# Performance work log

Hardware: AMD Instinct MI355X
Metric: run time of the kernel (lower is better)

Reference implementation:

```python
import jax, jax.numpy as jnp
import numpy as np

NUM_BANDS = 8
WINDOW = 2048
OVERLAP = 1024
SR = 16000


def _band_mask(L):
    # Replicates torch: band = searchsorted(band_ranges, |freq|, left) - 1.
    # DC bin gives band=-1 which torch negative-indexes into the LAST band,
    # hence the mod. All bins satisfy band < NUM_BANDS, so all are assigned.
    freqs = np.fft.fftfreq(L, 1.0 / SR)
    ranges = np.linspace(0.0, SR / 2.0, NUM_BANDS + 1)
    idx = np.searchsorted(ranges, np.abs(freqs), side='left') - 1
    idx = idx % NUM_BANDS
    mask = (idx[None, :] == np.arange(NUM_BANDS)[:, None]).astype(np.float32)
    return jnp.asarray(mask)  # [bands, L]


def _band_signals(x):
    # mag*exp(i*phase) of masked bins == masked complex bins; ifft().real per band
    L = x.shape[-1]
    X = jnp.fft.fft(x)                         # [B, L] complex
    mask = _band_mask(L)                       # [bands, L]
    Xb = X[:, None, :] * mask[None, :, :]      # [B, bands, L]
    return jnp.fft.ifft(Xb).real               # [B, bands, L]


def _chunks(sig):
    L = sig.shape[-1]
    hop = WINDOW - OVERLAP
    n = (L - OVERLAP) // hop                   # num_chunks (static)
    idx = (jnp.arange(n) * hop)[:, None] + jnp.arange(WINDOW)[None, :]  # [n, W]
    return sig[:, :, idx]                       # [B, bands, n, W]


def _loudness(x):
    # BS.1770-style energy loudness (vectorized stand-in for the repo's
    # undefined `loudness` helper): -0.691 + 10*log10(mean square)
    ms = jnp.mean(x * x, axis=-1)
    return -0.691 + 10.0 * jnp.log10(ms + 1e-12)


def reference(watermarked_signals, original_signals):
    ro = _band_signals(original_signals)
    rw = _band_signals(watermarked_signals)
    lo = _loudness(_chunks(ro))                # [B, bands, n]
    lw = _loudness(_chunks(rw))
    lo = jnp.where(jnp.isnan(lo), 0.0, lo)
    lw = jnp.where(jnp.isnan(lw), 0.0, lw)
    diff = (lw - lo).reshape(-1)               # ordered (i, j, k) like the torch loop
    w = jax.nn.softmax(diff)
    return jnp.sum(w * diff)


def setup_inputs() -> dict:
    key = jax.random.key(0)
    k1, k2 = jax.random.split(key)
    B, L = 8, 160000
    return {
        'watermarked_signals': jax.random.normal(k1, (B, L), dtype=jnp.float32),
        'original_signals': jax.random.normal(k2, (B, L), dtype=jnp.float32),
    }
```

## Files before the change

kernel.cpp:

```cpp
#include <hip/hip_runtime.h>
#include <math.h>

constexpr int L      = 160000;
constexpr int BATCH  = 8;
constexpr int NB     = 8;
constexpr int NHOPS  = 156;
constexpr int NCHUNK = 155;
constexpr int RS     = 289;
constexpr float TWO_PI = 6.28318530717958647692f;

__device__ __forceinline__ float2 cmulf(float2 a, float2 b) {
  return make_float2(a.x * b.x - a.y * b.y, a.x * b.y + a.y * b.x);
}

__device__ __forceinline__ float2 cisf(float a) {
  float s, c;
  __sincosf(a, &s, &c);
  return make_float2(c, s);
}

__device__ __forceinline__ int pad8(int i) { return i + (i >> 3); }

template <int SIGN>
__device__ __forceinline__ void bf4s(float2* v) {
  float2 t0 = make_float2(v[0].x + v[2].x, v[0].y + v[2].y);
  float2 t1 = make_float2(v[0].x - v[2].x, v[0].y - v[2].y);
  float2 t2 = make_float2(v[1].x + v[3].x, v[1].y + v[3].y);
  float2 t3 = make_float2(v[1].x - v[3].x, v[1].y - v[3].y);
  v[0] = make_float2(t0.x + t2.x, t0.y + t2.y);
  v[2] = make_float2(t0.x - t2.x, t0.y - t2.y);
  if constexpr (SIGN < 0) {
    v[1] = make_float2(t1.x + t3.y, t1.y - t3.x);
    v[3] = make_float2(t1.x - t3.y, t1.y + t3.x);
  } else {
    v[1] = make_float2(t1.x - t3.y, t1.y + t3.x);
    v[3] = make_float2(t1.x + t3.y, t1.y - t3.x);
  }
}

template <int SIGN>
__device__ __forceinline__ void bf5s(float2* v) {
  const float c1 = 0.30901699437494745f, s1 = 0.9510565162951535f;
  const float c2 = -0.8090169943749475f, s2 = 0.5877852522924731f;
  float2 t1 = make_float2(v[1].x + v[4].x, v[1].y + v[4].y);
  float2 t3 = make_float2(v[1].x - v[4].x, v[1].y - v[4].y);
  float2 t2 = make_float2(v[2].x + v[3].x, v[2].y + v[3].y);
  float2 t4 = make_float2(v[2].x - v[3].x, v[2].y - v[3].y);
  float2 a = make_float2(v[0].x + c1 * t1.x + c2 * t2.x, v[0].y + c1 * t1.y + c2 * t2.y);
  float2 b = make_float2(s1 * t3.x + s2 * t4.x, s1 * t3.y + s2 * t4.y);
  float2 c = make_float2(v[0].x + c2 * t1.x + c1 * t2.x, v[0].y + c2 * t1.y + c1 * t2.y);
  float2 d = make_float2(s2 * t3.x - s1 * t4.x, s2 * t3.y - s1 * t4.y);
  v[0] = make_float2(v[0].x + t1.x + t2.x, v[0].y + t1.y + t2.y);
  if constexpr (SIGN < 0) {
    v[1] = make_float2(a.x + b.y, a.y - b.x);
    v[4] = make_float2(a.x - b.y, a.y + b.x);
    v[2] = make_float2(c.x + d.y, c.y - d.x);
    v[3] = make_float2(c.x - d.y, c.y + d.x);
  } else {
    v[1] = make_float2(a.x - b.y, a.y + b.x);
    v[4] = make_float2(a.x + b.y, a.y - b.x);
    v[2] = make_float2(c.x - d.y, c.y + d.x);
    v[3] = make_float2(c.x + d.y, c.y - d.x);
  }
}

template <int R>
__device__ __forceinline__ void twchain(float2* v, float2 t1) {
  float2 t = t1;
  v[1] = cmulf(v[1], t);
#pragma unroll
  for (int r = 2; r < R; ++r) { t = cmulf(t, t1); v[r] = cmulf(v[r], t); }
}

__device__ __forceinline__ int rev3_5(int q) {
  int q5 = q / 5, q25 = q / 25;
  int d0 = q - 5 * q5, d1 = q5 - 5 * q25;
  return 25 * d0 + 5 * d1 + q25;
}

__device__ __forceinline__ int rev3_4(int q) {
  return ((q & 3) << 4) | (q & 12) | (q >> 4);
}

template <int SUB, int SIGN>
__device__ __forceinline__ void dif5_ip_stage_c(float2* a, int ln) {
  int i1 = ln, i2 = ln + 64;
  bool g2 = (i2 < 125);
  int j1 = i1 % SUB, j2 = i2 % SUB;
  int b1 = (i1 / SUB) * (5 * SUB) + j1;
  int b2 = (i2 / SUB) * (5 * SUB) + j2;
  float2 u[5], v[5];
#pragma unroll
  for (int r = 0; r < 5; ++r) u[r] = a[b1 + SUB * r];
  if (g2) {
#pragma unroll
    for (int r = 0; r < 5; ++r) v[r] = a[b2 + SUB * r];
  }
  bf5s<SIGN>(u);
  twchain<5>(u, cisf((float)SIGN * (TWO_PI / (float)(5 * SUB)) * (float)j1));
  if (g2) {
    bf5s<SIGN>(v);
    twchain<5>(v, cisf((float)SIGN * (TWO_PI / (float)(5 * SUB)) * (float)j2));
  }
#pragma unroll
  for (int r = 0; r < 5; ++r) a[b1 + SUB * r] = u[r];
  if (g2) {
#pragma unroll
    for (int r = 0; r < 5; ++r) a[b2 + SUB * r] = v[r];
  }
}

template <int SUB>
__device__ __forceinline__ void dif5_ip_stage_t(float2* a, int ln, float2 t1a, float2 t1b) {
  int i1 = ln, i2 = ln + 64;
  bool g2 = (i2 < 125);
  int j1 = i1 % SUB, j2 = i2 % SUB;
  int b1 = (i1 / SUB) * (5 * SUB) + j1;
  int b2 = (i2 / SUB) * (5 * SUB) + j2;
  float2 u[5], v[5];
#pragma unroll
  for (int r = 0; r < 5; ++r) u[r] = a[b1 + SUB * r];
  if (g2) {
#pragma unroll
    for (int r = 0; r < 5; ++r) v[r] = a[b2 + SUB * r];
  }
  bf5s<1>(u);
  twchain<5>(u, t1a);
  if (g2) {
    bf5s<1>(v);
    twchain<5>(v, t1b);
  }
#pragma unroll
  for (int r = 0; r < 5; ++r) a[b1 + SUB * r] = u[r];
  if (g2) {
#pragma unroll
    for (int r = 0; r < 5; ++r) a[b2 + SUB * r] = v[r];
  }
}

template <int SIGN>
__device__ __forceinline__ void dif625_ip(float2* a, int ln) {
  dif5_ip_stage_c<125, SIGN>(a, ln);
  dif5_ip_stage_c<25, SIGN>(a, ln);
  dif5_ip_stage_c<5, SIGN>(a, ln);
  int q1 = ln, q2 = ln + 64;
  bool g2 = (q2 < 125);
  float2 u[5], v[5];
#pragma unroll
  for (int r = 0; r < 5; ++r) u[r] = a[5 * q1 + r];
  if (g2) {
#pragma unroll
    for (int r = 0; r < 5; ++r) v[r] = a[5 * q2 + r];
  }
  bf5s<SIGN>(u);
  if (g2) bf5s<SIGN>(v);
  int rv1 = rev3_5(q1), rv2 = rev3_5(q2);
#pragma unroll
  for (int r = 0; r < 5; ++r) a[125 * r + rv1] = u[r];
  if (g2) {
#pragma unroll
    for (int r = 0; r < 5; ++r) a[125 * r + rv2] = v[r];
  }
}

template <int SIGN>
__device__ __forceinline__ void dif256sw_ip(float2* a, int ln) {
  {
    float2 u[4];
#pragma unroll
    for (int r = 0; r < 4; ++r) u[r] = a[pad8(ln + 64 * r)];
    bf4s<SIGN>(u);
    twchain<4>(u, cisf((float)SIGN * (TWO_PI / 256.0f) * (float)ln));
#pragma unroll
    for (int r = 0; r < 4; ++r) a[pad8(ln + 64 * r)] = u[r];
  }
  {
    int j = ln & 15, b = 64 * (ln >> 4) + j;
    float2 u[4];
#pragma unroll
    for (int r = 0; r < 4; ++r) u[r] = a[pad8(b + 16 * r)];
    bf4s<SIGN>(u);
    twchain<4>(u, cisf((float)SIGN * (TWO_PI / 64.0f) * (float)j));
#pragma unroll
    for (int r = 0; r < 4; ++r) a[pad8(b + 16 * r)] = u[r];
  }
  {
    int j = ln & 3, b = 16 * (ln >> 2) + j;
    float2 u[4];
#pragma unroll
    for (int r = 0; r < 4; ++r) u[r] = a[pad8(b + 4 * r)];
    bf4s<SIGN>(u);
    twchain<4>(u, cisf((float)SIGN * (TWO_PI / 16.0f) * (float)j));
#pragma unroll
    for (int r = 0; r < 4; ++r) a[pad8(b + 4 * r)] = u[r];
  }
  {
    float2 u[4];
#pragma unroll
    for (int r = 0; r < 4; ++r) u[r] = a[pad8(4 * ln + r)];
    bf4s<SIGN>(u);
    int rv = rev3_4(ln);
#pragma unroll
    for (int r = 0; r < 4; ++r) a[pad8(64 * r + rv)] = u[r];
  }
}

__global__ __launch_bounds__(256) void f1_kernel(const float* __restrict__ win,
                                                 const float* __restrict__ oin,
                                                 float2* __restrict__ G,
                                                 float* __restrict__ E) {
  __shared__ float2 A[4 * 625];
  int blk = blockIdx.x;
  int gid = blk * 256 + threadIdx.x;
  if (gid < 2 * BATCH * NB * NHOPS) E[gid] = 0.0f;
  int sig = blk >> 6, g = blk & 63;
  int n1base = g * 4;
  int tid = threadIdx.x;
  const float4* wp4 = (const float4*)(win + (size_t)sig * L);
  const float4* op4 = (const float4*)(oin + (size_t)sig * L);
  for (int r = tid; r < 625; r += 256) {
    float4 wv = wp4[r * 64 + g];
    float4 ov = op4[r * 64 + g];
    A[0 * 625 + r] = make_float2(wv.x, ov.x);
    A[1 * 625 + r] = make_float2(wv.y, ov.y);
    A[2 * 625 + r] = make_float2(wv.z, ov.z);
    A[3 * 625 + r] = make_float2(wv.w, ov.w);
  }
  __syncthreads();
  int wv_ = tid >> 6, ln = tid & 63;
  dif625_ip<-1>(A + wv_ * 625, ln);
  __syncthreads();
  int cc = tid & 3, k20 = tid >> 2;
  int n1 = n1base + cc;
  float w = -(TWO_PI / (float)L) * (float)n1;
  float2 t = cisf(w * (float)k20);
  float2 stp = cisf(w * 64.0f);
  for (int k2 = k20; k2 < 625; k2 += 64) {
    G[(size_t)sig * L + k2 * 256 + n1] = cmulf(A[cc * 625 + k2], t);
    t = cmulf(t, stp);
  }
}

__global__ __launch_bounds__(256) void f2_kernel(const float2* __restrict__ G,
                                                 float2* __restrict__ X) {
  __shared__ float2 A[4 * RS];
  int blk = blockIdx.x;
  int sig = blk / 157, gr = blk % 157;
  int k2base = gr * 4;
  int tid = threadIdx.x;
  int wv = tid >> 6, ln = tid & 63;
  int k2 = k2base + wv;
  float2* a = A + wv * RS;
  if (k2 < 625) {
#pragma unroll
    for (int r = 0; r < 4; ++r)
      a[pad8(ln + 64 * r)] = G[(size_t)sig * L + k2 * 256 + ln + 64 * r];
    dif256sw_ip<-1>(a, ln);
  }
  __syncthreads();
  for (int idx = tid; idx < 1024; idx += 256) {
    int row = idx >> 8, k1 = idx & 255;
    int k2e = k2base + row;
    if (k2e < 625) X[(size_t)sig * L + k2e * 256 + k1] = A[row * RS + pad8(k1)];
  }
}

__global__ __launch_bounds__(1024) void i1_kernel(const float2* __restrict__ X,
                                                  float2* __restrict__ H) {
  __shared__ float2 A[16 * RS];
  int blk = blockIdx.x;
  int gr = blk % 40, sb = blk / 40;
  int band = sb & 7, sig = sb >> 3;
  int k2base = gr * 16;
  int tid = threadIdx.x;
  int wv = tid >> 6, ln = tid & 63;
  int lo1, hi1, lo2, hi2;
  if (band < 7) {
    lo1 = 10000 * band + 1;        hi1 = 10000 * (band + 1);
    lo2 = L - 10000 * (band + 1);  hi2 = L - 10000 * band - 1;
  } else {
    lo1 = 70001; hi1 = 80000; lo2 = 80001; hi2 = 89999;
  }
  float2 zero = make_float2(0.0f, 0.0f);
  int k2 = k2base + wv;
  float2* row = A + wv * RS;
  for (int k1 = ln; k1 < 256; k1 += 64) row[pad8(k1)] = zero;
  if (k2 < 625) {
    const float2* Xr = X + (size_t)sig * L + k2 * 256;
    int s1 = (lo1 - k2 + 624) / 625;
    int e1 = (hi1 - k2) / 625; if (e1 > 255) e1 = 255;
    int s2 = (lo2 - k2 + 624) / 625;
    int e2 = (hi2 - k2) / 625; if (e2 > 255) e2 = 255;
    int c1 = e1 - s1 + 1;
    int c2 = e2 - s2 + 1;
    if (ln < c1) { int k1 = s1 + ln; row[pad8(k1)] = Xr[k1]; }
    int l2 = ln - 32;
    if (l2 >= 0 && l2 < c2) { int k1 = s2 + l2; row[pad8(k1)] = Xr[k1]; }
    if (band == 7 && k2 == 0 && ln == 0) row[pad8(0)] = Xr[0];
    dif256sw_ip<1>(row, ln);
  }
  __syncthreads();
  size_t obase = (size_t)(sig * NB + band) * L;
  int cc = tid & 15, n1g = tid >> 4;
  int k2e = k2base + cc;
  if (k2e < 625) {
    float a0 = (TWO_PI / (float)L) * (float)k2e;
    float2 t = cisf(a0 * (float)n1g);
    float2 stp = cisf(a0 * 64.0f);
#pragma unroll
    for (int it = 0; it < 4; ++it) {
      int n1 = n1g + 64 * it;
      H[obase + (size_t)n1 * 625 + k2e] = cmulf(A[cc * RS + pad8(n1)], t);
      t = cmulf(t, stp);
    }
  }
}

__global__ __launch_bounds__(256) void i2_kernel(const float2* __restrict__ H,
                                                 float* __restrict__ E) {
  __shared__ float2 A[4 * 625];
  __shared__ float P[4 * 2 * NHOPS];
  int blk = blockIdx.x;
  int g = blk & 31, sb = blk >> 5;
  int band = sb & 7, sig = sb >> 3;
  int tid = threadIdx.x;
  int wv = tid >> 6, ln = tid & 63;
  size_t base = (size_t)(sig * NB + band) * L;
  int n1A = 8 * g + wv, n1B = 8 * g + 4 + wv;
  const float2* HA = H + base + (size_t)n1A * 625;
  const float2* HB = H + base + (size_t)n1B * 625;
  int j1 = ln, j2 = ln + 64;
  bool g2 = (j2 < 125);
  float2 uA1[5], uA2[5], uB1[5], uB2[5];
#pragma unroll
  for (int r = 0; r < 5; ++r) uA1[r] = HA[j1 + 125 * r];
  if (g2) {
#pragma unroll
    for (int r = 0; r < 5; ++r) uA2[r] = HA[j2 + 125 * r];
  }
#pragma unroll
  for (int r = 0; r < 5; ++r) uB1[r] = HB[j1 + 125 * r];
  if (g2) {
#pragma unroll
    for (int r = 0; r < 5; ++r) uB2[r] = HB[j2 + 125 * r];
  }
  float2 tS1a = cisf((TWO_PI / 625.0f) * (float)j1);
  float2 tS1b = cisf((TWO_PI / 625.0f) * (float)j2);
  float2 tS2a = cisf((TWO_PI / 125.0f) * (float)(j1 % 25));
  float2 tS2b = cisf((TWO_PI / 125.0f) * (float)(j2 % 25));
  float2 tS3a = cisf((TWO_PI / 25.0f) * (float)(j1 % 5));
  float2 tS3b = cisf((TWO_PI / 25.0f) * (float)(j2 % 5));
  float2* a = A + wv * 625;
  float* Pw = P + wv * (2 * NHOPS);

  bf5s<1>(uA1);
  twchain<5>(uA1, tS1a);
#pragma unroll
  for (int r = 0; r < 5; ++r) a[j1 + 125 * r] = uA1[r];
  if (g2) {
    bf5s<1>(uA2);
    twchain<5>(uA2, tS1b);
#pragma unroll
    for (int r = 0; r < 5; ++r) a[j2 + 125 * r] = uA2[r];
  }
  dif5_ip_stage_t<25>(a, ln, tS2a, tS2b);
  dif5_ip_stage_t<5>(a, ln, tS3a, tS3b);
  {
    float2 u[5], v[5];
#pragma unroll
    for (int r = 0; r < 5; ++r) u[r] = a[5 * j1 + r];
    if (g2) {
#pragma unroll
      for (int r = 0; r < 5; ++r) v[r] = a[5 * j2 + r];
    }
    bf5s<1>(u);
    if (g2) bf5s<1>(v);
    int rv1 = rev3_5(j1), rv2 = rev3_5(j2);
#pragma unroll
    for (int r = 0; r < 5; ++r) a[125 * r + rv1] = u[r];
    if (g2) {
#pragma unroll
      for (int r = 0; r < 5; ++r) a[125 * r + rv2] = v[r];
    }
  }
  for (int h = ln; h < NHOPS; h += 64) {
    float ex = 0.0f, ey = 0.0f;
#pragma unroll
    for (int d = 0; d < 4; ++d) {
      float2 z = a[4 * h + d];
      ex += z.x * z.x;
      ey += z.y * z.y;
    }
    Pw[h] = ex;
    Pw[NHOPS + h] = ey;
  }

  bf5s<1>(uB1);
  twchain<5>(uB1, tS1a);
#pragma unroll
  for (int r = 0; r < 5; ++r) a[j1 + 125 * r] = uB1[r];
  if (g2) {
    bf5s<1>(uB2);
    twchain<5>(uB2, tS1b);
#pragma unroll
    for (int r = 0; r < 5; ++r) a[j2 + 125 * r] = uB2[r];
  }
  dif5_ip_stage_t<25>(a, ln, tS2a, tS2b);
  dif5_ip_stage_t<5>(a, ln, tS3a, tS3b);
  {
    float2 u[5], v[5];
#pragma unroll
    for (int r = 0; r < 5; ++r) u[r] = a[5 * j1 + r];
    if (g2) {
#pragma unroll
      for (int r = 0; r < 5; ++r) v[r] = a[5 * j2 + r];
    }
    bf5s<1>(u);
    if (g2) bf5s<1>(v);
    int rv1 = rev3_5(j1), rv2 = rev3_5(j2);
#pragma unroll
    for (int r = 0; r < 5; ++r) a[125 * r + rv1] = u[r];
    if (g2) {
#pragma unroll
      for (int r = 0; r < 5; ++r) a[125 * r + rv2] = v[r];
    }
  }
  for (int h = ln; h < NHOPS; h += 64) {
    float ex = 0.0f, ey = 0.0f;
#pragma unroll
    for (int d = 0; d < 4; ++d) {
      float2 z = a[4 * h + d];
      ex += z.x * z.x;
      ey += z.y * z.y;
    }
    Pw[h] += ex;
    Pw[NHOPS + h] += ey;
  }
  __syncthreads();
  int eb = (sig * NB + band) * NHOPS;
  for (int idx = tid; idx < 2 * NHOPS; idx += 256) {
    float v = P[idx] + P[2 * NHOPS + idx] + P[4 * NHOPS + idx] + P[6 * NHOPS + idx];
    int comp = idx / NHOPS, h = idx - comp * NHOPS;
    atomicAdd(&E[comp * (BATCH * NB * NHOPS) + eb + h], v);
  }
}

__global__ __launch_bounds__(1024) void finalize_kernel(const float* __restrict__ E,
                                                        float* __restrict__ out) {
  constexpr int ND = BATCH * NB * NCHUNK;
  constexpr float SC = (1.0f / 2048.0f) / ((float)L * (float)L);
  __shared__ float diffs[ND];
  __shared__ float sred[1024];
  int tid = threadIdx.x;
  for (int idx = tid; idx < ND; idx += 1024) {
    int sb = idx / NCHUNK;
    int k = idx - sb * NCHUNK;
    float msw = (E[sb * NHOPS + k] + E[sb * NHOPS + k + 1]) * SC;
    float mso = (E[64 * NHOPS + sb * NHOPS + k] + E[64 * NHOPS + sb * NHOPS + k + 1]) * SC;
    float lw = -0.691f + 10.0f * log10f(msw + 1e-12f);
    float lo = -0.691f + 10.0f * log10f(mso + 1e-12f);
    diffs[idx] = lw - lo;
  }
  __syncthreads();
  float mx = -3.4e38f;
  for (int idx = tid; idx < ND; idx += 1024) mx = fmaxf(mx, diffs[idx]);
  sred[tid] = mx;
  __syncthreads();
  for (int s = 512; s > 0; s >>= 1) {
    if (tid < s) sred[tid] = fmaxf(sred[tid], sred[tid + s]);
    __syncthreads();
  }
  float gmax = sred[0];
  __syncthreads();
  float se = 0.0f, swd = 0.0f;
  for (int idx = tid; idx < ND; idx += 1024) {
    float d = diffs[idx];
    float e = expf(d - gmax);
    se += e;
    swd += d * e;
  }
  sred[tid] = se; __syncthreads();
  for (int s = 512; s > 0; s >>= 1) { if (tid < s) sred[tid] += sred[tid + s]; __syncthreads(); }
  float tot = sred[0];
  __syncthreads();
  sred[tid] = swd; __syncthreads();
  for (int s = 512; s > 0; s >>= 1) { if (tid < s) sred[tid] += sred[tid + s]; __syncthreads(); }
  if (tid == 0) out[0] = sred[0] / tot;
}

extern "C" void kernel_launch(void* const* d_in, const int* in_sizes, int n_in,
                              void* d_out, int out_size, void* d_ws, size_t ws_size,
                              hipStream_t stream) {
  (void)in_sizes; (void)n_in; (void)out_size; (void)ws_size;
  char* ws = (char*)d_ws;
  float2* G = (float2*)ws;
  float2* X = (float2*)(ws + 10240000);
  float2* H = (float2*)(ws + 20480000);
  float*  E = (float*)(ws + 102400000);
  const float* w = (const float*)d_in[0];
  const float* o = (const float*)d_in[1];

  f1_kernel<<<dim3(BATCH * 64), dim3(256), 0, stream>>>(w, o, G, E);
  f2_kernel<<<dim3(BATCH * 157), dim3(256), 0, stream>>>(G, X);
  i1_kernel<<<dim3(BATCH * NB * 40), dim3(1024), 0, stream>>>(X, H);
  i2_kernel<<<dim3(BATCH * NB * 32), dim3(256), 0, stream>>>(H, E);
  finalize_kernel<<<dim3(1), dim3(1024), 0, stream>>>(E, (float*)d_out);
}
```

Before: 149.8 us.

## Store band intermediate in fp16 and transpose G layout for coalesced writes

The large per-band intermediate H written by i1 and read by i2 is now stored as half2 instead of float2, pre-scaled by 1/L so the values fit fp16 range, and the finalize scale is adjusted to match. This halves the dominant memory traffic between those two kernels. Separately, f1 now writes G in an n1-major layout with contiguous rows, and f2 is rebuilt with 1024-thread blocks that gather 16 columns into shared memory before their FFTs. The fp16 storage reduces precision of the band spectra, which may affect accuracy of the loudness differences.

```diff
diff --git a/kernel.cpp b/kernel.cpp
--- a/kernel.cpp
+++ b/kernel.cpp
@@ -1,4 +1,5 @@
 #include <hip/hip_runtime.h>
+#include <hip/hip_fp16.h>
 #include <math.h>
 
 constexpr int L      = 160000;
@@ -8,6 +9,7 @@
 constexpr int NCHUNK = 155;
 constexpr int RS     = 289;
 constexpr float TWO_PI = 6.28318530717958647692f;
+constexpr float INVL = 1.0f / (float)L;
 
 __device__ __forceinline__ float2 cmulf(float2 a, float2 b) {
   return make_float2(a.x * b.x - a.y * b.y, a.x * b.y + a.y * b.x);
@@ -230,35 +232,38 @@
   int wv_ = tid >> 6, ln = tid & 63;
   dif625_ip<-1>(A + wv_ * 625, ln);
   __syncthreads();
-  int cc = tid & 3, k20 = tid >> 2;
-  int n1 = n1base + cc;
+  int n1 = n1base + wv_;
   float w = -(TWO_PI / (float)L) * (float)n1;
-  float2 t = cisf(w * (float)k20);
+  float2 t = cisf(w * (float)ln);
   float2 stp = cisf(w * 64.0f);
-  for (int k2 = k20; k2 < 625; k2 += 64) {
-    G[(size_t)sig * L + k2 * 256 + n1] = cmulf(A[cc * 625 + k2], t);
+  float2* Gr = G + (size_t)sig * L + (size_t)n1 * 625;
+  const float2* Ar = A + wv_ * 625;
+  for (int k2 = ln; k2 < 625; k2 += 64) {
+    Gr[k2] = cmulf(Ar[k2], t);
     t = cmulf(t, stp);
   }
 }
 
-__global__ __launch_bounds__(256) void f2_kernel(const float2* __restrict__ G,
-                                                 float2* __restrict__ X) {
-  __shared__ float2 A[4 * RS];
+__global__ __launch_bounds__(1024) void f2_kernel(const float2* __restrict__ G,
+                                                  float2* __restrict__ X) {
+  __shared__ float2 A[16 * RS];
   int blk = blockIdx.x;
-  int sig = blk / 157, gr = blk % 157;
-  int k2base = gr * 4;
+  int sig = blk / 40, gr = blk % 40;
+  int k2base = gr * 16;
   int tid = threadIdx.x;
   int wv = tid >> 6, ln = tid & 63;
+  for (int idx = tid; idx < 4096; idx += 1024) {
+    int n1 = idx >> 4, cc = idx & 15;
+    int k2 = k2base + cc;
+    if (k2 < 625)
+      A[cc * RS + pad8(n1)] = G[(size_t)sig * L + (size_t)n1 * 625 + k2];
+  }
+  __syncthreads();
   int k2 = k2base + wv;
   float2* a = A + wv * RS;
-  if (k2 < 625) {
-#pragma unroll
-    for (int r = 0; r < 4; ++r)
-      a[pad8(ln + 64 * r)] = G[(size_t)sig * L + k2 * 256 + ln + 64 * r];
-    dif256sw_ip<-1>(a, ln);
-  }
-  __syncthreads();
-  for (int idx = tid; idx < 1024; idx += 256) {
+  if (k2 < 625) dif256sw_ip<-1>(a, ln);
+  __syncthreads();
+  for (int idx = tid; idx < 4096; idx += 1024) {
     int row = idx >> 8, k1 = idx & 255;
     int k2e = k2base + row;
     if (k2e < 625) X[(size_t)sig * L + k2e * 256 + k1] = A[row * RS + pad8(k1)];
@@ -266,7 +271,7 @@
 }
 
 __global__ __launch_bounds__(1024) void i1_kernel(const float2* __restrict__ X,
-                                                  float2* __restrict__ H) {
+                                                  __half2* __restrict__ H) {
   __shared__ float2 A[16 * RS];
   int blk = blockIdx.x;
   int gr = blk % 40, sb = blk / 40;
@@ -310,13 +315,14 @@
 #pragma unroll
     for (int it = 0; it < 4; ++it) {
       int n1 = n1g + 64 * it;
-      H[obase + (size_t)n1 * 625 + k2e] = cmulf(A[cc * RS + pad8(n1)], t);
+      float2 val = cmulf(A[cc * RS + pad8(n1)], t);
+      H[obase + (size_t)n1 * 625 + k2e] = __floats2half2_rn(val.x * INVL, val.y * INVL);
       t = cmulf(t, stp);
     }
   }
 }
 
-__global__ __launch_bounds__(256) void i2_kernel(const float2* __restrict__ H,
+__global__ __launch_bounds__(256) void i2_kernel(const __half2* __restrict__ H,
                                                  float* __restrict__ E) {
   __shared__ float2 A[4 * 625];
   __shared__ float P[4 * 2 * NHOPS];
@@ -327,22 +333,22 @@
   int wv = tid >> 6, ln = tid & 63;
   size_t base = (size_t)(sig * NB + band) * L;
   int n1A = 8 * g + wv, n1B = 8 * g + 4 + wv;
-  const float2* HA = H + base + (size_t)n1A * 625;
-  const float2* HB = H + base + (size_t)n1B * 625;
+  const __half2* HA = H + base + (size_t)n1A * 625;
+  const __half2* HB = H + base + (size_t)n1B * 625;
   int j1 = ln, j2 = ln + 64;
   bool g2 = (j2 < 125);
-  float2 uA1[5], uA2[5], uB1[5], uB2[5];
-#pragma unroll
-  for (int r = 0; r < 5; ++r) uA1[r] = HA[j1 + 125 * r];
-  if (g2) {
-#pragma unroll
-    for (int r = 0; r < 5; ++r) uA2[r] = HA[j2 + 125 * r];
-  }
-#pragma unroll
-  for (int r = 0; r < 5; ++r) uB1[r] = HB[j1 + 125 * r];
-  if (g2) {
-#pragma unroll
-    for (int r = 0; r < 5; ++r) uB2[r] = HB[j2 + 125 * r];
+  __half2 hA1[5], hA2[5], hB1[5], hB2[5];
+#pragma unroll
+  for (int r = 0; r < 5; ++r) hA1[r] = HA[j1 + 125 * r];
+  if (g2) {
+#pragma unroll
+    for (int r = 0; r < 5; ++r) hA2[r] = HA[j2 + 125 * r];
+  }
+#pragma unroll
+  for (int r = 0; r < 5; ++r) hB1[r] = HB[j1 + 125 * r];
+  if (g2) {
+#pragma unroll
+    for (int r = 0; r < 5; ++r) hB2[r] = HB[j2 + 125 * r];
   }
   float2 tS1a = cisf((TWO_PI / 625.0f) * (float)j1);
   float2 tS1b = cisf((TWO_PI / 625.0f) * (float)j2);
@@ -353,15 +359,23 @@
   float2* a = A + wv * 625;
   float* Pw = P + wv * (2 * NHOPS);
 
-  bf5s<1>(uA1);
-  twchain<5>(uA1, tS1a);
-#pragma unroll
-  for (int r = 0; r < 5; ++r) a[j1 + 125 * r] = uA1[r];
-  if (g2) {
-    bf5s<1>(uA2);
-    twchain<5>(uA2, tS1b);
-#pragma unroll
-    for (int r = 0; r < 5; ++r) a[j2 + 125 * r] = uA2[r];
+  {
+    float2 u[5];
+#pragma unroll
+    for (int r = 0; r < 5; ++r) u[r] = __half22float2(hA1[r]);
+    bf5s<1>(u);
+    twchain<5>(u, tS1a);
+#pragma unroll
+    for (int r = 0; r < 5; ++r) a[j1 + 125 * r] = u[r];
+    if (g2) {
+      float2 v[5];
+#pragma unroll
+      for (int r = 0; r < 5; ++r) v[r] = __half22float2(hA2[r]);
+      bf5s<1>(v);
+      twchain<5>(v, tS1b);
+#pragma unroll
+      for (int r = 0; r < 5; ++r) a[j2 + 125 * r] = v[r];
+    }
   }
   dif5_ip_stage_t<25>(a, ln, tS2a, tS2b);
   dif5_ip_stage_t<5>(a, ln, tS3a, tS3b);
@@ -395,15 +409,23 @@
     Pw[NHOPS + h] = ey;
   }
 
-  bf5s<1>(uB1);
-  twchain<5>(uB1, tS1a);
-#pragma unroll
-  for (int r = 0; r < 5; ++r) a[j1 + 125 * r] = uB1[r];
-  if (g2) {
-    bf5s<1>(uB2);
-    twchain<5>(uB2, tS1b);
-#pragma unroll
-    for (int r = 0; r < 5; ++r) a[j2 + 125 * r] = uB2[r];
+  {
+    float2 u[5];
+#pragma unroll
+    for (int r = 0; r < 5; ++r) u[r] = __half22float2(hB1[r]);
+    bf5s<1>(u);
+    twchain<5>(u, tS1a);
+#pragma unroll
+    for (int r = 0; r < 5; ++r) a[j1 + 125 * r] = u[r];
+    if (g2) {
+      float2 v[5];
+#pragma unroll
+      for (int r = 0; r < 5; ++r) v[r] = __half22float2(hB2[r]);
+      bf5s<1>(v);
+      twchain<5>(v, tS1b);
+#pragma unroll
+      for (int r = 0; r < 5; ++r) a[j2 + 125 * r] = v[r];
+    }
   }
   dif5_ip_stage_t<25>(a, ln, tS2a, tS2b);
   dif5_ip_stage_t<5>(a, ln, tS3a, tS3b);
@@ -448,7 +470,7 @@
 __global__ __launch_bounds__(1024) void finalize_kernel(const float* __restrict__ E,
                                                         float* __restrict__ out) {
   constexpr int ND = BATCH * NB * NCHUNK;
-  constexpr float SC = (1.0f / 2048.0f) / ((float)L * (float)L);
+  constexpr float SC = 1.0f / 2048.0f;
   __shared__ float diffs[ND];
   __shared__ float sred[1024];
   int tid = threadIdx.x;
@@ -493,15 +515,15 @@
                               hipStream_t stream) {
   (void)in_sizes; (void)n_in; (void)out_size; (void)ws_size;
   char* ws = (char*)d_ws;
-  float2* G = (float2*)ws;
-  float2* X = (float2*)(ws + 10240000);
-  float2* H = (float2*)(ws + 20480000);
-  float*  E = (float*)(ws + 102400000);
+  float2*  G = (float2*)ws;
+  float2*  X = (float2*)(ws + 10240000);
+  __half2* H = (__half2*)(ws + 20480000);
+  float*   E = (float*)(ws + 61440000);
   const float* w = (const float*)d_in[0];
   const float* o = (const float*)d_in[1];
 
   f1_kernel<<<dim3(BATCH * 64), dim3(256), 0, stream>>>(w, o, G, E);
-  f2_kernel<<<dim3(BATCH * 157), dim3(256), 0, stream>>>(G, X);
+  f2_kernel<<<dim3(BATCH * 40), dim3(1024), 0, stream>>>(G, X);
   i1_kernel<<<dim3(BATCH * NB * 40), dim3(1024), 0, stream>>>(X, H);
   i2_kernel<<<dim3(BATCH * NB * 32), dim3(256), 0, stream>>>(H, E);
   finalize_kernel<<<dim3(1), dim3(1024), 0, stream>>>(E, (float*)d_out);
```

Measured after the change: 151.2 us. Within noise of the previous version (+0.9%).
